# Kernel tuning notes

Hardware: AMD Instinct MI355X
Metric: run time of the kernel (lower is better)

Reference implementation:

```python
import jax, jax.numpy as jnp
import numpy as np

N = 50000   # num_nodes
E = 600000  # num_edges (avg degree 12)
D = 128     # feats_dim


def setup_inputs() -> dict:
    key = jax.random.key(0)
    ks = jax.random.split(key, 10)
    s = 1.0 / np.sqrt(D)
    return {
        "node_ids": jnp.arange(N, dtype=jnp.int32),
        "edge_src": jax.random.randint(ks[0], (E,), 0, N, dtype=jnp.int32),
        "edge_dst": jax.random.randint(ks[1], (E,), 0, N, dtype=jnp.int32),
        "edge_weight": jax.random.uniform(ks[2], (E,), dtype=jnp.float32),
        "emb": jax.random.normal(ks[3], (N, D), dtype=jnp.float32),
        "W_self1": jax.random.uniform(ks[4], (D, D), jnp.float32, -s, s),
        "W_neigh1": jax.random.uniform(ks[5], (D, D), jnp.float32, -s, s),
        "b1": jnp.zeros((D,), jnp.float32),
        "W_self2": jax.random.uniform(ks[6], (D, D), jnp.float32, -s, s),
        "W_neigh2": jax.random.uniform(ks[7], (D, D), jnp.float32, -s, s),
        "b2": jnp.zeros((D,), jnp.float32),
    }


def _sage_conv(h, src, dst, w, W_self, W_neigh, b):
    # DGL SAGEConv('mean') with edge_weight: neigh = mean_in(w_e * h_src)
    msg = h[src] * w[:, None]                                  # [E, D] gather
    neigh_sum = jax.ops.segment_sum(msg, dst, num_segments=N)  # [N, D] scatter-add
    deg = jax.ops.segment_sum(jnp.ones_like(w), dst, num_segments=N)
    neigh = neigh_sum / jnp.maximum(deg, 1.0)[:, None]         # 0 for isolated nodes
    # fc_self carries the bias, fc_neigh has none (DGL convention)
    return h @ W_self.T + b + neigh @ W_neigh.T


def reference(node_ids, edge_src, edge_dst, edge_weight, emb,
              W_self1, W_neigh1, b1, W_self2, W_neigh2, b2):
    h = emb[node_ids]                                          # embedding lookup
    h = _sage_conv(h, edge_src, edge_dst, edge_weight, W_self1, W_neigh1, b1)
    h = jax.nn.relu(h)
    h = _sage_conv(h, edge_src, edge_dst, edge_weight, W_self2, W_neigh2, b2)
    return h
```

## Files before the change

### kernel.cpp

```cpp
#include <hip/hip_runtime.h>
#include <stdint.h>

#define DIM 128
#define SCAN_BLOCKS 256
#define CP 16

typedef __attribute__((ext_vector_type(8))) short bf16x8;
typedef __attribute__((ext_vector_type(4))) float floatx4;

__device__ __forceinline__ float bf2f(unsigned short u) {
    union { unsigned int i; float f; } v; v.i = ((unsigned int)u) << 16; return v.f;
}
__device__ __forceinline__ unsigned short f2bf(float f) {
    union { float f; unsigned int i; } v; v.f = f;
    unsigned int r = (v.i + 0x7FFFu + ((v.i >> 16) & 1u)) >> 16;
    return (unsigned short)r;
}

__device__ __forceinline__ int block_flag(const unsigned int* __restrict__ emb32) {
    __shared__ int sf;
    if (threadIdx.x < 64) {
        unsigned int v = emb32[threadIdx.x];
        float f = bf2f((unsigned short)(v & 0xffffu));
        int bad = !(fabsf(f) < 1e4f);
        unsigned long long m = __ballot(bad);
        if (threadIdx.x == 0) sf = (__popcll(m) > 16) ? 1 : 0;
    }
    __syncthreads();
    return sf;
}


__global__ void hist_kernel(const int* __restrict__ dst, int* __restrict__ cnt, int E) {
    int base = (blockIdx.x * 256 + threadIdx.x) * 4;
#pragma unroll
    for (int i = 0; i < 4; ++i) {
        int e = base + i;
        if (e < E) atomicAdd(&cnt[dst[e] * CP], 1);
    }
}

__global__ __launch_bounds__(256) void scan_partial(const int* __restrict__ cnt,
                                                    int* __restrict__ partials, int N) {
    int b = blockIdx.x;
    int chunk = (N + gridDim.x - 1) / gridDim.x;
    int beg = b * chunk;
    int end = min(beg + chunk, N);
    int t = threadIdx.x;
    int s = 0;
    for (int i = beg + t; i < end; i += 256) s += cnt[i * CP];
    for (int off = 32; off > 0; off >>= 1) s += __shfl_xor(s, off);
    __shared__ int ws[4];
    if ((t & 63) == 0) ws[t >> 6] = s;
    __syncthreads();
    if (t == 0) partials[b] = ws[0] + ws[1] + ws[2] + ws[3];
}

__global__ __launch_bounds__(256) void scan_final(int* __restrict__ cnt,
                                                  int* __restrict__ row_ptr,
                                                  const int* __restrict__ partials, int N) {
    __shared__ int ptile[256];
    __shared__ int tile[256];
    __shared__ int s_run;
    int t = threadIdx.x;
    int b = blockIdx.x;
    int pv = partials[t];
    ptile[t] = pv;
    __syncthreads();
    for (int off = 1; off < 256; off <<= 1) {
        int x = (t >= off) ? ptile[t - off] : 0;
        __syncthreads();
        ptile[t] += x;
        __syncthreads();
    }
    if (t == b) s_run = ptile[t] - pv;
    __syncthreads();

    int chunk = (N + gridDim.x - 1) / gridDim.x;
    int beg = b * chunk;
    int end = min(beg + chunk, N);
    for (int base = beg; base < end; base += 256) {
        int i = base + t;
        int v = (i < end) ? cnt[i * CP] : 0;
        tile[t] = v;
        __syncthreads();
        for (int off = 1; off < 256; off <<= 1) {
            int x = (t >= off) ? tile[t - off] : 0;
            __syncthreads();
            tile[t] += x;
            __syncthreads();
        }
        int run = s_run;
        if (i < end) {
            int start = run + tile[t] - v;
            row_ptr[i] = start;
            cnt[i * CP] = start;
            if (i == N - 1) row_ptr[N] = start + v;
        }
        __syncthreads();
        if (t == 255) s_run = run + tile[255];
        __syncthreads();
    }
}

__global__ __launch_bounds__(256) void scatter_prep_kernel(
        const int* __restrict__ src, const int* __restrict__ dst,
        const void* __restrict__ w_any,
        int* __restrict__ cursor, unsigned int* __restrict__ s_edge, int E,
        const void* __restrict__ s0, const void* __restrict__ s1,
        const void* __restrict__ s2, const void* __restrict__ s3,
        const void* __restrict__ s4, const void* __restrict__ s5,
        unsigned short* __restrict__ wcat,
        const int* __restrict__ ids, const void* __restrict__ emb,
        unsigned int* __restrict__ h032,
        int scat_blocks, int conv_blocks, int total_gather) {
    int flag = block_flag((const unsigned int*)emb);
    const int W = DIM * DIM;
    int blk = (int)blockIdx.x;
    if (blk < scat_blocks) {
        int e = blk * 256 + threadIdx.x;
        if (e >= E) return;
        unsigned short wb = flag ? f2bf(((const float*)w_any)[e])
                                 : ((const unsigned short*)w_any)[e];
        int d = dst[e];
        unsigned int rec = ((unsigned int)src[e] & 0xffffu) | ((unsigned int)wb << 16);
        int pos = atomicAdd(&cursor[d * CP], 1);
        __builtin_nontemporal_store(rec, &s_edge[pos]);
    } else if (blk < scat_blocks + conv_blocks) {
        int i = (blk - scat_blocks) * 256 + threadIdx.x;
        const void* srcp; int off;
        if      (i < W)             { srcp = s0; off = i; }
        else if (i < 2 * W)         { srcp = s1; off = i - W; }
        else if (i < 3 * W)         { srcp = s2; off = i - 2 * W; }
        else if (i < 4 * W)         { srcp = s3; off = i - 3 * W; }
        else if (i < 4 * W + DIM)   { srcp = s4; off = i - 4 * W; }
        else if (i < 4 * W + 2*DIM) { srcp = s5; off = i - 4 * W - DIM; }
        else return;
        wcat[i] = flag ? f2bf(((const float*)srcp)[off])
                       : ((const unsigned short*)srcp)[off];
    } else {
        int t = (blk - scat_blocks - conv_blocks) * 256 + threadIdx.x;
        if (t >= total_gather) return;
        int n = t >> 6;
        int f = t & 63;
        int id = ids[n];
        unsigned int o;
        if (flag) {
            const float* e = (const float*)emb + (size_t)id * DIM + f * 2;
            o = ((unsigned int)f2bf(e[1]) << 16) | (unsigned int)f2bf(e[0]);
        } else {
            o = ((const unsigned int*)emb)[(size_t)id * 64 + f];
        }
        h032[t] = o;
    }
}


__global__ __launch_bounds__(256) void agg_kernel(const uint2* __restrict__ h64,
                                                  const int* __restrict__ row_ptr,
                                                  const unsigned int* __restrict__ s_edge,
                                                  uint2* __restrict__ out64,
                                                  int N, int E) {
    int lane = threadIdx.x & 63;
    int half = lane >> 5;
    int sub  = lane & 31;
    int node = blockIdx.x * 8 + (threadIdx.x >> 6) * 2 + half;
    if (node >= N) return;
    int beg = max(row_ptr[node], 0);
    int end = min(row_ptr[node + 1], E);
    float a0 = 0.f, a1 = 0.f, a2 = 0.f, a3 = 0.f;
    int e = beg;
    for (; e + 8 <= end; e += 8) {
        unsigned int r[8]; int k[8]; float w[8]; uint2 v[8];
#pragma unroll
        for (int i = 0; i < 8; ++i) r[i] = s_edge[e + i];
#pragma unroll
        for (int i = 0; i < 8; ++i) {
            k[i] = min((int)(r[i] & 0xffffu), N - 1);
            w[i] = bf2f((unsigned short)(r[i] >> 16));
        }
#pragma unroll
        for (int i = 0; i < 8; ++i) v[i] = h64[(size_t)k[i] * 32 + sub];
#pragma unroll
        for (int i = 0; i < 8; ++i) {
            a0 += w[i] * bf2f((unsigned short)(v[i].x & 0xffffu));
            a1 += w[i] * bf2f((unsigned short)(v[i].x >> 16));
            a2 += w[i] * bf2f((unsigned short)(v[i].y & 0xffffu));
            a3 += w[i] * bf2f((unsigned short)(v[i].y >> 16));
        }
    }
    for (; e + 4 <= end; e += 4) {
        unsigned int r[4]; int k[4]; float w[4]; uint2 v[4];
#pragma unroll
        for (int i = 0; i < 4; ++i) r[i] = s_edge[e + i];
#pragma unroll
        for (int i = 0; i < 4; ++i) {
            k[i] = min((int)(r[i] & 0xffffu), N - 1);
            w[i] = bf2f((unsigned short)(r[i] >> 16));
        }
#pragma unroll
        for (int i = 0; i < 4; ++i) v[i] = h64[(size_t)k[i] * 32 + sub];
#pragma unroll
        for (int i = 0; i < 4; ++i) {
            a0 += w[i] * bf2f((unsigned short)(v[i].x & 0xffffu));
            a1 += w[i] * bf2f((unsigned short)(v[i].x >> 16));
            a2 += w[i] * bf2f((unsigned short)(v[i].y & 0xffffu));
            a3 += w[i] * bf2f((unsigned short)(v[i].y >> 16));
        }
    }
    for (; e < end; ++e) {
        unsigned int r = s_edge[e];
        int k = min((int)(r & 0xffffu), N - 1);
        float w = bf2f((unsigned short)(r >> 16));
        uint2 v = h64[(size_t)k * 32 + sub];
        a0 += w * bf2f((unsigned short)(v.x & 0xffffu));
        a1 += w * bf2f((unsigned short)(v.x >> 16));
        a2 += w * bf2f((unsigned short)(v.y & 0xffffu));
        a3 += w * bf2f((unsigned short)(v.y >> 16));
    }
    float inv = (end > beg) ? 1.0f / (float)(end - beg) : 0.f;
    a0 *= inv; a1 *= inv; a2 *= inv; a3 *= inv;
    uint2 o;
    o.x = ((unsigned int)f2bf(a1) << 16) | (unsigned int)f2bf(a0);
    o.y = ((unsigned int)f2bf(a3) << 16) | (unsigned int)f2bf(a2);
    out64[(size_t)node * 32 + sub] = o;
}


#define WROW 68

__global__ __launch_bounds__(256) void gemm_layer(const unsigned short* __restrict__ A0,
                                                  const unsigned short* __restrict__ A1,
                                                  const unsigned short* __restrict__ W0,
                                                  const unsigned short* __restrict__ W1,
                                                  const unsigned short* __restrict__ bias,
                                                  void* __restrict__ out,
                                                  const unsigned int* __restrict__ emb32,
                                                  int n_rows, int relu, int is_final) {
    __shared__ unsigned int lw[2 * DIM * WROW];
    int fp32_out = is_final ? block_flag(emb32) : (void(block_flag(emb32)), 0);
    int t = threadIdx.x;

#pragma unroll
    for (int mat = 0; mat < 2; ++mat) {
        const uint4* src = (const uint4*)(mat ? W1 : W0);
        unsigned int* dstl = lw + mat * DIM * WROW;
#pragma unroll
        for (int i = 0; i < 8; ++i) {
            int c = i * 256 + t;
            uint4 v = src[c];
            *(uint4*)&dstl[(c >> 4) * WROW + (c & 15) * 4] = v;
        }
    }
    __syncthreads();

    int wave = t >> 6;
    int lane = t & 63;
    int quad = lane >> 4;
    int l16  = lane & 15;
    int m_base = blockIdx.x * 128 + wave * 32;

    floatx4 acc0[8], acc1[8];
#pragma unroll
    for (int c = 0; c < 8; ++c) {
        acc0[c] = (floatx4){0.f, 0.f, 0.f, 0.f};
        acc1[c] = (floatx4){0.f, 0.f, 0.f, 0.f};
    }

    int r0 = min(m_base + l16, n_rows - 1);
    int r1 = min(m_base + 16 + l16, n_rows - 1);

#pragma unroll
    for (int mat = 0; mat < 2; ++mat) {
        const unsigned short* A  = mat ? A1 : A0;
        const unsigned int* lwm = lw + mat * DIM * WROW;
        const unsigned short* Ar0 = A + (size_t)r0 * DIM;
        const unsigned short* Ar1 = A + (size_t)r1 * DIM;
#pragma unroll
        for (int ks = 0; ks < 4; ++ks) {
            int k0 = ks * 32 + quad * 8;
            bf16x8 a0 = *(const bf16x8*)(Ar0 + k0);
            bf16x8 a1 = *(const bf16x8*)(Ar1 + k0);
#pragma unroll
            for (int c = 0; c < 8; ++c) {
                bf16x8 b = *(const bf16x8*)&lwm[(c * 16 + l16) * WROW + (k0 >> 1)];
                acc0[c] = __builtin_amdgcn_mfma_f32_16x16x32_bf16(a0, b, acc0[c], 0, 0, 0);
                acc1[c] = __builtin_amdgcn_mfma_f32_16x16x32_bf16(a1, b, acc1[c], 0, 0, 0);
            }
        }
    }

#pragma unroll
    for (int c = 0; c < 8; ++c) {
        int col = c * 16 + l16;
        float bv = bf2f(bias[col]);
#pragma unroll
        for (int r = 0; r < 4; ++r) {
            int row0 = m_base + quad * 4 + r;
            int row1 = row0 + 16;
            if (row0 < n_rows) {
                float v = acc0[c][r] + bv;
                if (relu) v = fmaxf(v, 0.f);
                size_t idx = (size_t)row0 * DIM + col;
                if (fp32_out) ((float*)out)[idx] = v;
                else          ((unsigned short*)out)[idx] = f2bf(v);
            }
            if (row1 < n_rows) {
                float v = acc1[c][r] + bv;
                if (relu) v = fmaxf(v, 0.f);
                size_t idx = (size_t)row1 * DIM + col;
                if (fp32_out) ((float*)out)[idx] = v;
                else          ((unsigned short*)out)[idx] = f2bf(v);
            }
        }
    }
}


extern "C" void kernel_launch(void* const* d_in, const int* in_sizes, int n_in,
                              void* d_out, int out_size, void* d_ws, size_t ws_size,
                              hipStream_t stream) {
    const int* node_ids = (const int*)d_in[0];
    const int* edge_src = (const int*)d_in[1];
    const int* edge_dst = (const int*)d_in[2];
    const void* edge_w  = d_in[3];
    const void* emb     = d_in[4];
    const void* Ws1     = d_in[5];
    const void* Wn1     = d_in[6];
    const void* b1      = d_in[7];
    const void* Ws2     = d_in[8];
    const void* Wn2     = d_in[9];
    const void* b2      = d_in[10];

    const int N = in_sizes[0];
    const int E = in_sizes[1];

    char* w = (char*)d_ws;
    auto alloc = [&](size_t bytes) {
        char* p = w;
        w += (bytes + 255) & ~(size_t)255;
        return p;
    };
    int* partials       = (int*)alloc((size_t)SCAN_BLOCKS * 4);
    int* row_ptr        = (int*)alloc((size_t)(N + 1) * 4);
    int* cnt            = (int*)alloc((size_t)N * CP * 4);
    const int W = DIM * DIM;
    unsigned short* wcat = (unsigned short*)alloc((size_t)(4 * W + 2 * DIM) * 2);
    unsigned short* Ws1c = wcat;
    unsigned short* Wn1c = wcat + W;
    unsigned short* Ws2c = wcat + 2 * W;
    unsigned short* Wn2c = wcat + 3 * W;
    unsigned short* b1c  = wcat + 4 * W;
    unsigned short* b2c  = wcat + 4 * W + DIM;
    unsigned int* s_edge = (unsigned int*)alloc((size_t)E * 4);
    unsigned short* h0  = (unsigned short*)alloc((size_t)N * DIM * 2);
    unsigned short* h1  = (unsigned short*)alloc((size_t)N * DIM * 2);
    unsigned short* ngh = (unsigned short*)alloc((size_t)N * DIM * 2);

    const unsigned int* emb32 = (const unsigned int*)emb;

    hipMemsetAsync(cnt, 0, (size_t)N * CP * 4, stream);
    hist_kernel<<<(E + 1023) / 1024, 256, 0, stream>>>(edge_dst, cnt, E);
    scan_partial<<<SCAN_BLOCKS, 256, 0, stream>>>(cnt, partials, N);
    scan_final<<<SCAN_BLOCKS, 256, 0, stream>>>(cnt, row_ptr, partials, N);

    const int CN = 4 * W + 2 * DIM;
    const int scat_blocks = (E + 255) / 256;
    const int conv_blocks = (CN + 255) / 256;
    const int gather_total = N * 64;
    const int gather_blocks = (gather_total + 255) / 256;
    scatter_prep_kernel<<<scat_blocks + conv_blocks + gather_blocks, 256, 0, stream>>>(
        edge_src, edge_dst, edge_w, cnt, s_edge, E,
        Ws1, Wn1, Ws2, Wn2, b1, b2, wcat, node_ids, emb,
        (unsigned int*)h0, scat_blocks, conv_blocks, gather_total);

    agg_kernel<<<(N + 7) / 8, 256, 0, stream>>>((const uint2*)h0, row_ptr,
                                                s_edge, (uint2*)ngh, N, E);
    gemm_layer<<<(N + 127) / 128, 256, 0, stream>>>(h0, ngh, Ws1c, Wn1c, b1c,
                                                    h1, emb32, N, 1, 0);

    agg_kernel<<<(N + 7) / 8, 256, 0, stream>>>((const uint2*)h1, row_ptr,
                                                s_edge, (uint2*)ngh, N, E);
    gemm_layer<<<(N + 127) / 128, 256, 0, stream>>>(h1, ngh, Ws2c, Wn2c, b2c,
                                                    d_out, emb32, N, 0, 1);
}
```

Before: 245.7 us.

## Build CSR with two-level bucket sort using shared-memory atomics

Replaces the global-atomic histogram, padded count array, two-pass scan and global-atomic scatter with a two-level counting sort. Edges are first bucketed by the high byte of the destination using per-block shared histograms and offsets, then each bucket block builds its row pointers and final order with shared-memory atomics. This removes the memset and the contended global atomics on a padded counter array. In exchange it adds intermediate buffers, an extra pass over the edges and more kernel launches. The bucket index is masked to 8 bits, so it assumes fewer than 65536 nodes.

Measured after the change: 215.2 us. 1.14x faster.

```diff
diff --git a/kernel.cpp b/kernel.cpp
--- a/kernel.cpp
+++ b/kernel.cpp
@@ -2,8 +2,6 @@
 #include <stdint.h>
 
 #define DIM 128
-#define SCAN_BLOCKS 256
-#define CP 16
 
 typedef __attribute__((ext_vector_type(8))) short bf16x8;
 typedef __attribute__((ext_vector_type(4))) float floatx4;
@@ -31,103 +29,129 @@
 }
 
 
-__global__ void hist_kernel(const int* __restrict__ dst, int* __restrict__ cnt, int E) {
-    int base = (blockIdx.x * 256 + threadIdx.x) * 4;
-#pragma unroll
-    for (int i = 0; i < 4; ++i) {
-        int e = base + i;
-        if (e < E) atomicAdd(&cnt[dst[e] * CP], 1);
-    }
-}
-
-__global__ __launch_bounds__(256) void scan_partial(const int* __restrict__ cnt,
-                                                    int* __restrict__ partials, int N) {
-    int b = blockIdx.x;
-    int chunk = (N + gridDim.x - 1) / gridDim.x;
-    int beg = b * chunk;
-    int end = min(beg + chunk, N);
-    int t = threadIdx.x;
-    int s = 0;
-    for (int i = beg + t; i < end; i += 256) s += cnt[i * CP];
-    for (int off = 32; off > 0; off >>= 1) s += __shfl_xor(s, off);
-    __shared__ int ws[4];
-    if ((t & 63) == 0) ws[t >> 6] = s;
-    __syncthreads();
-    if (t == 0) partials[b] = ws[0] + ws[1] + ws[2] + ws[3];
-}
-
-__global__ __launch_bounds__(256) void scan_final(int* __restrict__ cnt,
-                                                  int* __restrict__ row_ptr,
-                                                  const int* __restrict__ partials, int N) {
-    __shared__ int ptile[256];
+__global__ __launch_bounds__(256) void bucket_hist(const int* __restrict__ dst,
+                                                   int* __restrict__ bcnt, int E, int NB) {
+    __shared__ int cnt[256];
+    int t = threadIdx.x, j = blockIdx.x;
+    cnt[t] = 0;
+    __syncthreads();
+    int chunk = (E + 255) / 256;
+    int beg = j * chunk;
+    int end = min(beg + chunk, E);
+    for (int e = beg + t; e < end; e += 256) atomicAdd(&cnt[(dst[e] >> 8) & 255], 1);
+    __syncthreads();
+    if (t < NB) bcnt[j * NB + t] = cnt[t];
+}
+
+__global__ __launch_bounds__(256) void bucket_scan(const int* __restrict__ bcnt,
+                                                   int* __restrict__ boff,
+                                                   int* __restrict__ btot, int NB) {
     __shared__ int tile[256];
-    __shared__ int s_run;
-    int t = threadIdx.x;
-    int b = blockIdx.x;
-    int pv = partials[t];
-    ptile[t] = pv;
+    int t = threadIdx.x, k = blockIdx.x;
+    int v = bcnt[t * NB + k];
+    tile[t] = v;
     __syncthreads();
     for (int off = 1; off < 256; off <<= 1) {
-        int x = (t >= off) ? ptile[t - off] : 0;
-        __syncthreads();
-        ptile[t] += x;
-        __syncthreads();
-    }
-    if (t == b) s_run = ptile[t] - pv;
-    __syncthreads();
-
-    int chunk = (N + gridDim.x - 1) / gridDim.x;
-    int beg = b * chunk;
-    int end = min(beg + chunk, N);
-    for (int base = beg; base < end; base += 256) {
-        int i = base + t;
-        int v = (i < end) ? cnt[i * CP] : 0;
-        tile[t] = v;
-        __syncthreads();
-        for (int off = 1; off < 256; off <<= 1) {
-            int x = (t >= off) ? tile[t - off] : 0;
-            __syncthreads();
-            tile[t] += x;
-            __syncthreads();
-        }
-        int run = s_run;
-        if (i < end) {
-            int start = run + tile[t] - v;
-            row_ptr[i] = start;
-            cnt[i * CP] = start;
-            if (i == N - 1) row_ptr[N] = start + v;
-        }
-        __syncthreads();
-        if (t == 255) s_run = run + tile[255];
-        __syncthreads();
-    }
-}
-
-__global__ __launch_bounds__(256) void scatter_prep_kernel(
+        int x = (t >= off) ? tile[t - off] : 0;
+        __syncthreads();
+        tile[t] += x;
+        __syncthreads();
+    }
+    boff[t * NB + k] = tile[t] - v;
+    if (t == 255) btot[k] = tile[255];
+}
+
+__global__ __launch_bounds__(256) void bucket_scatter(
         const int* __restrict__ src, const int* __restrict__ dst,
-        const void* __restrict__ w_any,
-        int* __restrict__ cursor, unsigned int* __restrict__ s_edge, int E,
+        const void* __restrict__ w_any, const unsigned int* __restrict__ emb32,
+        const int* __restrict__ boff, const int* __restrict__ btot,
+        unsigned int* __restrict__ s_tmp, unsigned char* __restrict__ s_tmpb,
+        int E, int NB) {
+    int flag = block_flag(emb32);
+    __shared__ int bs[256];
+    __shared__ int cursor[256];
+    int t = threadIdx.x, j = blockIdx.x;
+    int bv = (t < NB) ? btot[t] : 0;
+    bs[t] = bv;
+    __syncthreads();
+    for (int off = 1; off < 256; off <<= 1) {
+        int x = (t >= off) ? bs[t - off] : 0;
+        __syncthreads();
+        bs[t] += x;
+        __syncthreads();
+    }
+    cursor[t] = (bs[t] - bv) + ((t < NB) ? boff[j * NB + t] : 0);
+    __syncthreads();
+    int chunk = (E + 255) / 256;
+    int beg = j * chunk;
+    int end = min(beg + chunk, E);
+    for (int e = beg + t; e < end; e += 256) {
+        int d = dst[e];
+        unsigned short wb = flag ? f2bf(((const float*)w_any)[e])
+                                 : ((const unsigned short*)w_any)[e];
+        unsigned int rec = ((unsigned int)src[e] & 0xffffu) | ((unsigned int)wb << 16);
+        int pos = atomicAdd(&cursor[(d >> 8) & 255], 1);
+        s_tmp[pos] = rec;
+        s_tmpb[pos] = (unsigned char)(d & 255);
+    }
+}
+
+__global__ __launch_bounds__(256) void bucket_csr(
+        const int* __restrict__ btot,
+        const unsigned int* __restrict__ s_tmp, const unsigned char* __restrict__ s_tmpb,
+        unsigned int* __restrict__ s_edge, int* __restrict__ row_ptr, int N, int NB) {
+    __shared__ int bs[256];
+    __shared__ int hist[256];
+    __shared__ int cur[256];
+    int t = threadIdx.x, b = blockIdx.x;
+    int bv = (t < NB) ? btot[t] : 0;
+    bs[t] = bv;
+    __syncthreads();
+    for (int off = 1; off < 256; off <<= 1) {
+        int x = (t >= off) ? bs[t - off] : 0;
+        __syncthreads();
+        bs[t] += x;
+        __syncthreads();
+    }
+    int myEnd = bs[b];
+    int myStart = myEnd - btot[b];
+    hist[t] = 0;
+    __syncthreads();
+    for (int e = myStart + t; e < myEnd; e += 256) atomicAdd(&hist[s_tmpb[e]], 1);
+    __syncthreads();
+    int hv = hist[t];
+    for (int off = 1; off < 256; off <<= 1) {
+        int x = (t >= off) ? hist[t - off] : 0;
+        __syncthreads();
+        hist[t] += x;
+        __syncthreads();
+    }
+    int rowstart = myStart + hist[t] - hv;
+    int node = b * 256 + t;
+    if (node < N) row_ptr[node] = rowstart;
+    if (b == NB - 1 && t == 0) row_ptr[N] = myEnd;
+    cur[t] = rowstart;
+    __syncthreads();
+    for (int e = myStart + t; e < myEnd; e += 256) {
+        unsigned int rec = s_tmp[e];
+        int pos = atomicAdd(&cur[s_tmpb[e]], 1);
+        s_edge[pos] = rec;
+    }
+}
+
+__global__ __launch_bounds__(256) void prep_kernel(
         const void* __restrict__ s0, const void* __restrict__ s1,
         const void* __restrict__ s2, const void* __restrict__ s3,
         const void* __restrict__ s4, const void* __restrict__ s5,
         unsigned short* __restrict__ wcat,
         const int* __restrict__ ids, const void* __restrict__ emb,
         unsigned int* __restrict__ h032,
-        int scat_blocks, int conv_blocks, int total_gather) {
+        int conv_blocks, int total_gather) {
     int flag = block_flag((const unsigned int*)emb);
     const int W = DIM * DIM;
     int blk = (int)blockIdx.x;
-    if (blk < scat_blocks) {
-        int e = blk * 256 + threadIdx.x;
-        if (e >= E) return;
-        unsigned short wb = flag ? f2bf(((const float*)w_any)[e])
-                                 : ((const unsigned short*)w_any)[e];
-        int d = dst[e];
-        unsigned int rec = ((unsigned int)src[e] & 0xffffu) | ((unsigned int)wb << 16);
-        int pos = atomicAdd(&cursor[d * CP], 1);
-        __builtin_nontemporal_store(rec, &s_edge[pos]);
-    } else if (blk < scat_blocks + conv_blocks) {
-        int i = (blk - scat_blocks) * 256 + threadIdx.x;
+    if (blk < conv_blocks) {
+        int i = blk * 256 + threadIdx.x;
         const void* srcp; int off;
         if      (i < W)             { srcp = s0; off = i; }
         else if (i < 2 * W)         { srcp = s1; off = i - W; }
@@ -139,7 +163,7 @@
         wcat[i] = flag ? f2bf(((const float*)srcp)[off])
                        : ((const unsigned short*)srcp)[off];
     } else {
-        int t = (blk - scat_blocks - conv_blocks) * 256 + threadIdx.x;
+        int t = (blk - conv_blocks) * 256 + threadIdx.x;
         if (t >= total_gather) return;
         int n = t >> 6;
         int f = t & 63;
@@ -334,6 +358,7 @@
 
     const int N = in_sizes[0];
     const int E = in_sizes[1];
+    const int NB = (N + 255) >> 8;
 
     char* w = (char*)d_ws;
     auto alloc = [&](size_t bytes) {
@@ -341,9 +366,10 @@
         w += (bytes + 255) & ~(size_t)255;
         return p;
     };
-    int* partials       = (int*)alloc((size_t)SCAN_BLOCKS * 4);
+    int* bcnt           = (int*)alloc((size_t)256 * NB * 4);
+    int* boff           = (int*)alloc((size_t)256 * NB * 4);
+    int* btot           = (int*)alloc((size_t)256 * 4);
     int* row_ptr        = (int*)alloc((size_t)(N + 1) * 4);
-    int* cnt            = (int*)alloc((size_t)N * CP * 4);
     const int W = DIM * DIM;
     unsigned short* wcat = (unsigned short*)alloc((size_t)(4 * W + 2 * DIM) * 2);
     unsigned short* Ws1c = wcat;
@@ -352,6 +378,8 @@
     unsigned short* Wn2c = wcat + 3 * W;
     unsigned short* b1c  = wcat + 4 * W;
     unsigned short* b2c  = wcat + 4 * W + DIM;
+    unsigned int* s_tmp  = (unsigned int*)alloc((size_t)E * 4);
+    unsigned char* s_tmpb = (unsigned char*)alloc((size_t)E);
     unsigned int* s_edge = (unsigned int*)alloc((size_t)E * 4);
     unsigned short* h0  = (unsigned short*)alloc((size_t)N * DIM * 2);
     unsigned short* h1  = (unsigned short*)alloc((size_t)N * DIM * 2);
@@ -359,20 +387,19 @@
 
     const unsigned int* emb32 = (const unsigned int*)emb;
 
-    hipMemsetAsync(cnt, 0, (size_t)N * CP * 4, stream);
-    hist_kernel<<<(E + 1023) / 1024, 256, 0, stream>>>(edge_dst, cnt, E);
-    scan_partial<<<SCAN_BLOCKS, 256, 0, stream>>>(cnt, partials, N);
-    scan_final<<<SCAN_BLOCKS, 256, 0, stream>>>(cnt, row_ptr, partials, N);
+    bucket_hist<<<256, 256, 0, stream>>>(edge_dst, bcnt, E, NB);
+    bucket_scan<<<NB, 256, 0, stream>>>(bcnt, boff, btot, NB);
+    bucket_scatter<<<256, 256, 0, stream>>>(edge_src, edge_dst, edge_w, emb32,
+                                            boff, btot, s_tmp, s_tmpb, E, NB);
+    bucket_csr<<<NB, 256, 0, stream>>>(btot, s_tmp, s_tmpb, s_edge, row_ptr, N, NB);
 
     const int CN = 4 * W + 2 * DIM;
-    const int scat_blocks = (E + 255) / 256;
     const int conv_blocks = (CN + 255) / 256;
     const int gather_total = N * 64;
     const int gather_blocks = (gather_total + 255) / 256;
-    scatter_prep_kernel<<<scat_blocks + conv_blocks + gather_blocks, 256, 0, stream>>>(
-        edge_src, edge_dst, edge_w, cnt, s_edge, E,
+    prep_kernel<<<conv_blocks + gather_blocks, 256, 0, stream>>>(
         Ws1, Wn1, Ws2, Wn2, b1, b2, wcat, node_ids, emb,
-        (unsigned int*)h0, scat_blocks, conv_blocks, gather_total);
+        (unsigned int*)h0, conv_blocks, gather_total);
 
     agg_kernel<<<(N + 7) / 8, 256, 0, stream>>>((const uint2*)h0, row_ptr,
                                                 s_edge, (uint2*)ngh, N, E);
```
